# Kernel tuning notes

Hardware: AMD Instinct MI355X
Metric: run time of the kernel (lower is better)

Reference implementation:

```python
import jax, jax.numpy as jnp
import numpy as np

N_NODES = 50000
N_EDGES = 800000
D = 128


def _dense_params(key, d_in, d_out):
    kw, kb = jax.random.split(key)
    W = jax.random.normal(kw, (d_in, d_out), dtype=jnp.float32) / np.sqrt(d_in)
    b = jnp.zeros((d_out,), dtype=jnp.float32)
    return W, b


def setup_inputs() -> dict:
    key = jax.random.key(0)
    ks = jax.random.split(key, 9)
    nodes = jax.random.normal(ks[0], (N_NODES, D), dtype=jnp.float32)
    edges = jax.random.normal(ks[1], (N_EDGES, D), dtype=jnp.float32)
    senders = jax.random.randint(ks[2], (N_EDGES,), 0, N_NODES, dtype=jnp.int32)
    receivers = jax.random.randint(ks[3], (N_EDGES,), 0, N_NODES, dtype=jnp.int32)
    W_s1, b_s1 = _dense_params(ks[4], D, D)   # Dense on nodes -> sent_attributes_1
    W_r, b_r = _dense_params(ks[5], D, D)     # Dense on nodes -> received_attributes
    W_e, b_e = _dense_params(ks[6], D, D)     # Dense on edges
    W_att, b_att = _dense_params(ks[7], D, 1) # attention Dense -> scalar per edge
    W_m, b_m = _dense_params(ks[8], D, D)     # Dense on message (simple_update)
    return {
        "nodes": nodes, "edges": edges, "senders": senders, "receivers": receivers,
        "W_s1": W_s1, "b_s1": b_s1, "W_r": W_r, "b_r": b_r,
        "W_e": W_e, "b_e": b_e, "W_att": W_att, "b_att": b_att,
        "W_m": W_m, "b_m": b_m,
    }


def reference(nodes, edges, senders, receivers,
              W_s1, b_s1, W_r, b_r, W_e, b_e, W_att, b_att, W_m, b_m):
    n = nodes.shape[0]
    # dense projections on nodes, then gather along edges
    sent_1 = (nodes @ W_s1 + b_s1)[senders]          # [E, D]
    received = (nodes @ W_r + b_r)[receivers]        # [E, D]
    sent_2 = nodes[senders]                          # [E, D] (simple_update: raw gather)
    e_proj = edges @ W_e + b_e                       # [E, D]
    edges_new = sent_1 + e_proj + received           # add_features=True
    # attention: Dense(1) + leaky_relu, segment softmax over receivers
    att = jax.nn.leaky_relu(edges_new @ W_att + b_att)          # [E, 1]
    seg_max = jax.ops.segment_max(att, receivers, num_segments=n)
    expv = jnp.exp(att - seg_max[receivers])
    denom = jax.ops.segment_sum(expv, receivers, num_segments=n)
    weights = expv / denom[receivers]                            # [E, 1]
    # message: Dense on gathered sender features, weighted scatter-sum
    message = weights * (sent_2 @ W_m + b_m)                     # [E, D]
    nodes_new = jax.ops.segment_sum(message, receivers, num_segments=n)  # [N, D]
    return nodes_new, edges_new
```

## Files before the change

### kernel.cpp

```cpp
#include <hip/hip_runtime.h>
#include <hip/hip_bf16.h>
#include <cstdint>
#include <cstddef>

#define NN 50000
#define NE 800000
#define DD 128

typedef __attribute__((ext_vector_type(8))) short short8;
typedef __attribute__((ext_vector_type(4))) float f32x4;

__device__ __forceinline__ unsigned short f2bf(float f) {
  unsigned u = __float_as_uint(f);
  u = (u + 0x7FFFu + ((u >> 16) & 1u)) >> 16;
  return (unsigned short)u;
}

__global__ void k_prep(const float* __restrict__ Ws1, const float* __restrict__ Wr,
                       const float* __restrict__ Wm, const float* __restrict__ We,
                       unsigned short* __restrict__ Wt) {
  int i = blockIdx.x * blockDim.x + threadIdx.x;
  for (int idx = i; idx < 4 * DD * DD; idx += gridDim.x * blockDim.x) {
    int m = idx >> 14, r = idx & 16383, col = r >> 7, k = r & 127;
    const float* src = (m == 0) ? Ws1 : (m == 1) ? Wr : (m == 2) ? Wm : We;
    Wt[idx] = f2bf(src[k * DD + col]);
  }
}

__device__ __forceinline__ unsigned cvtpk(float lo, float hi) {
  unsigned r;
  asm("v_cvt_pk_bf16_f32 %0, %1, %2" : "=v"(r) : "v"(lo), "v"(hi));
  return r;
}

__device__ __forceinline__ short8 cvt8(f32x4 f0, f32x4 f1) {
  union { short8 s; unsigned u[4]; } t;
  t.u[0] = cvtpk(f0[0], f0[1]);
  t.u[1] = cvtpk(f0[2], f0[3]);
  t.u[2] = cvtpk(f1[0], f1[1]);
  t.u[3] = cvtpk(f1[2], f1[3]);
  return t.s;
}

__device__ __forceinline__ void stage_w(const unsigned short* __restrict__ Wt,
                                        char* __restrict__ lds, int tid) {
#pragma unroll
  for (int c = 0; c < 8; ++c) {
    int ci = tid * 8 + c;
    int col = ci >> 4, slot = ci & 15;
    uint4 v = *(const uint4*)(Wt + ci * 8);
    *(uint4*)(lds + col * 256 + ((slot ^ col) & 15) * 16) = v;
  }
}

__device__ __forceinline__ short8 read_w(const char* __restrict__ lds, int col, int slot) {
  return *(const short8*)(lds + col * 256 + ((slot ^ col) & 15) * 16);
}

__global__ __launch_bounds__(256, 4) void k_nodeproj(
    const float* __restrict__ nodes, const unsigned short* __restrict__ Wt,
    const float* __restrict__ b_s1, const float* __restrict__ b_r, const float* __restrict__ b_m,
    float* __restrict__ P1, float* __restrict__ Pr, float* __restrict__ Pm) {
  __shared__ char ldsW[32768];
  int m = blockIdx.y;
  int tid = threadIdx.x;
  stage_w(Wt + m * 16384, ldsW, tid);
  __syncthreads();
  const float* bias = (m == 0) ? b_s1 : (m == 1) ? b_r : b_m;
  float* P = (m == 0) ? P1 : (m == 1) ? Pr : Pm;
  int wid = tid >> 6, l = tid & 63;
  int lmod = l & 15, ldiv = l >> 4;
  int wave = blockIdx.x * 4 + wid, nw = gridDim.x * 4;
  for (int b = wave; b < NN / 16; b += nw) {
    int row = b * 16 + lmod;
    const float* nrow = nodes + (size_t)row * DD;
    short8 bb[4];
#pragma unroll
    for (int kk = 0; kk < 4; ++kk) {
      const f32x4* p = (const f32x4*)(nrow + kk * 32 + ldiv * 8);
      bb[kk] = cvt8(p[0], p[1]);
    }
    f32x4 acc[8] = {};
#pragma unroll
    for (int kk = 0; kk < 4; ++kk) {
#pragma unroll
      for (int rb = 0; rb < 8; ++rb) {
        short8 a = read_w(ldsW, rb * 16 + lmod, kk * 4 + ldiv);
        acc[rb] = __builtin_amdgcn_mfma_f32_16x16x32_bf16(a, bb[kk], acc[rb], 0, 0, 0);
      }
    }
    float* Prow = P + (size_t)row * DD;
#pragma unroll
    for (int rb = 0; rb < 8; ++rb) {
      int d0 = rb * 16 + ldiv * 4;
      f32x4 bv = *(const f32x4*)(bias + d0);
      f32x4 v = acc[rb];
#pragma unroll
      for (int j = 0; j < 4; ++j) v[j] += bv[j];
      *(f32x4*)(Prow + d0) = v;
    }
  }
}

__global__ __launch_bounds__(256, 4) void k_edge(
    const float* __restrict__ edges, const int* __restrict__ senders,
    const int* __restrict__ receivers, const unsigned short* __restrict__ WtE,
    const float* __restrict__ b_e, const float* __restrict__ P1, const float* __restrict__ Pr,
    const float* __restrict__ W_att, const float* __restrict__ b_att,
    float* __restrict__ out_edges, float* __restrict__ attb, int* __restrict__ cnt) {
  __shared__ char ldsW[32768];
  int tid = threadIdx.x;
  stage_w(WtE, ldsW, tid);
  __syncthreads();
  int wid = tid >> 6, l = tid & 63;
  int lmod = l & 15, ldiv = l >> 4;
  int wave = blockIdx.x * 4 + wid, nw = gridDim.x * 4;
  float batt = b_att[0];
  for (int b = wave; b < NE / 16; b += nw) {
    int e = b * 16 + lmod;
    const float* erow = edges + (size_t)e * DD;
    short8 bb[4];
#pragma unroll
    for (int kk = 0; kk < 4; ++kk) {
      const f32x4* p = (const f32x4*)(erow + kk * 32 + ldiv * 8);
      f32x4 f0 = __builtin_nontemporal_load(p);
      f32x4 f1 = __builtin_nontemporal_load(p + 1);
      bb[kk] = cvt8(f0, f1);
    }
    f32x4 acc[8] = {};
#pragma unroll
    for (int kk = 0; kk < 4; ++kk) {
#pragma unroll
      for (int rb = 0; rb < 8; ++rb) {
        short8 a = read_w(ldsW, rb * 16 + lmod, kk * 4 + ldiv);
        acc[rb] = __builtin_amdgcn_mfma_f32_16x16x32_bf16(a, bb[kk], acc[rb], 0, 0, 0);
      }
    }
    int s = senders[e], rc = receivers[e];
    const float* p1 = P1 + (size_t)s * DD;
    const float* pr = Pr + (size_t)rc * DD;
    float* oe = out_edges + (size_t)e * DD;
    float att = 0.f;
#pragma unroll
    for (int rb = 0; rb < 8; ++rb) {
      int d0 = rb * 16 + ldiv * 4;
      f32x4 g1 = *(const f32x4*)(p1 + d0);
      f32x4 gr = *(const f32x4*)(pr + d0);
      f32x4 be = *(const f32x4*)(b_e + d0);
      f32x4 wa = *(const f32x4*)(W_att + d0);
      f32x4 v = acc[rb];
#pragma unroll
      for (int j = 0; j < 4; ++j) {
        float x = v[j] + be[j] + g1[j] + gr[j];
        v[j] = x;
        att += x * wa[j];
      }
      __builtin_nontemporal_store(v, (f32x4*)(oe + d0));
    }
    att += __shfl_xor(att, 16);
    att += __shfl_xor(att, 32);
    if (ldiv == 0) {
      float av = att + batt;
      av = (av >= 0.f) ? av : 0.01f * av;
      attb[e] = av;
      atomicAdd(&cnt[rc], 1);
    }
  }
}

__global__ __launch_bounds__(1024) void k_scan(const int* __restrict__ cnt,
                                               int* __restrict__ offs) {
  __shared__ int wsum[16];
  __shared__ int sbase;
  int t = threadIdx.x;
  int lane = t & 63, wid = t >> 6;
  if (t == 0) { sbase = 0; offs[0] = 0; }
  __syncthreads();
  for (int c = 0; c < 13; ++c) {
    int i0 = c * 4096 + t * 4;
    int v0 = 0, v1 = 0, v2 = 0, v3 = 0;
    if (i0 + 3 < NN) {
      int4 v = *(const int4*)(cnt + i0);
      v0 = v.x; v1 = v.y; v2 = v.z; v3 = v.w;
    } else {
      if (i0 + 0 < NN) v0 = cnt[i0 + 0];
      if (i0 + 1 < NN) v1 = cnt[i0 + 1];
      if (i0 + 2 < NN) v2 = cnt[i0 + 2];
      if (i0 + 3 < NN) v3 = cnt[i0 + 3];
    }
    int p1 = v0, p2 = p1 + v1, p3 = p2 + v2, p4 = p3 + v3;
    int x = p4;
#pragma unroll
    for (int d = 1; d < 64; d <<= 1) {
      int o = __shfl_up(x, d, 64);
      if (lane >= d) x += o;
    }
    if (lane == 63) wsum[wid] = x;
    int excl_lane = x - p4;
    __syncthreads();
    int wbase = 0, tot = 0;
#pragma unroll
    for (int w2 = 0; w2 < 16; ++w2) {
      int sv = wsum[w2];
      if (w2 < wid) wbase += sv;
      tot += sv;
    }
    int base = sbase + wbase + excl_lane;
    if (i0 + 0 < NN) offs[i0 + 1] = base + p1;
    if (i0 + 1 < NN) offs[i0 + 2] = base + p2;
    if (i0 + 2 < NN) offs[i0 + 3] = base + p3;
    if (i0 + 3 < NN) offs[i0 + 4] = base + p4;
    __syncthreads();
    if (t == 0) sbase += tot;
    __syncthreads();
  }
}

__global__ void k_fill(const int* __restrict__ receivers, const int* __restrict__ offs,
                       int* __restrict__ cursor, int* __restrict__ eidx) {
  int e = blockIdx.x * 256 + threadIdx.x;
  if (e < NE) {
    int rc = receivers[e];
    int pos = offs[rc] + atomicAdd(&cursor[rc], 1);
    eidx[pos] = e;
  }
}

__global__ __launch_bounds__(256) void k_node(
    const int* __restrict__ offs, const int* __restrict__ eidx,
    const int* __restrict__ senders, const float* __restrict__ attb,
    const float* __restrict__ Pm, float* __restrict__ out_nodes) {
  int wid = threadIdx.x >> 6, l = threadIdx.x & 63;
  int n = blockIdx.x * 4 + wid;
  if (n >= NN) return;
  int start = offs[n], end = offs[n + 1];
  float m = -3.4e38f, denom = 0.f, ax = 0.f, ay = 0.f;
  for (int c = start; c < end; c += 64) {
    int rem = end - c;
    if (rem > 64) rem = 64;
    float a_l = -3.4e38f;
    int s_l = 0;
    if (l < rem) {
      int e = eidx[c + l];
      a_l = attb[e];
      s_l = senders[e];
    }
    float cm = a_l;
#pragma unroll
    for (int d = 1; d < 64; d <<= 1) cm = fmaxf(cm, __shfl_xor(cm, d));
    if (cm > m) {
      float sc = __expf(m - cm);
      denom *= sc; ax *= sc; ay *= sc;
      m = cm;
    }
#pragma unroll 4
    for (int i = 0; i < rem; ++i) {
      float a = __shfl(a_l, i);
      int s = __shfl(s_l, i);
      float w = __expf(a - m);
      denom += w;
      float2 v = *(const float2*)(Pm + (size_t)s * DD + l * 2);
      ax += w * v.x;
      ay += w * v.y;
    }
  }
  float2 o = {0.f, 0.f};
  if (end > start) {
    float inv = 1.f / denom;
    o.x = ax * inv;
    o.y = ay * inv;
  }
  *(float2*)(out_nodes + (size_t)n * DD + l * 2) = o;
}

extern "C" void kernel_launch(void* const* d_in, const int* in_sizes, int n_in,
                              void* d_out, int out_size, void* d_ws, size_t ws_size,
                              hipStream_t stream) {
  (void)in_sizes; (void)n_in; (void)out_size; (void)ws_size;
  const float* nodes = (const float*)d_in[0];
  const float* edges = (const float*)d_in[1];
  const int* senders = (const int*)d_in[2];
  const int* receivers = (const int*)d_in[3];
  const float* W_s1 = (const float*)d_in[4];
  const float* b_s1 = (const float*)d_in[5];
  const float* W_r = (const float*)d_in[6];
  const float* b_r = (const float*)d_in[7];
  const float* W_e = (const float*)d_in[8];
  const float* b_e = (const float*)d_in[9];
  const float* W_att = (const float*)d_in[10];
  const float* b_att = (const float*)d_in[11];
  const float* W_m = (const float*)d_in[12];
  const float* b_m = (const float*)d_in[13];

  float* out_nodes = (float*)d_out;
  float* out_edges = out_nodes + (size_t)NN * DD;

  char* w = (char*)d_ws;
  unsigned short* Wt = (unsigned short*)w; w += (size_t)4 * DD * DD * 2;
  float* P1 = (float*)w; w += (size_t)NN * DD * 4;
  float* Pr = (float*)w; w += (size_t)NN * DD * 4;
  float* Pm = (float*)w; w += (size_t)NN * DD * 4;
  float* attb = (float*)w; w += (size_t)NE * 4;
  int* eidx = (int*)w; w += (size_t)NE * 4;
  int* cnt = (int*)w; w += (size_t)NN * 4;
  int* cursor = (int*)w; w += (size_t)NN * 4;
  int* offs = (int*)w; w += (size_t)(NN + 1) * 4;

  hipMemsetAsync(cnt, 0, (size_t)NN * 8, stream);

  k_prep<<<64, 256, 0, stream>>>(W_s1, W_r, W_m, W_e, Wt);
  k_nodeproj<<<dim3(256, 3), 256, 0, stream>>>(nodes, Wt, b_s1, b_r, b_m, P1, Pr, Pm);
  k_edge<<<1024, 256, 0, stream>>>(edges, senders, receivers, Wt + 3 * 16384, b_e,
                                   P1, Pr, W_att, b_att, out_edges, attb, cnt);
  k_scan<<<1, 1024, 0, stream>>>(cnt, offs);
  k_fill<<<(NE + 255) / 256, 256, 0, stream>>>(receivers, offs, cursor, eidx);
  k_node<<<NN / 4, 256, 0, stream>>>(offs, eidx, senders, attb, Pm, out_nodes);
}
```

Before: 456.3 us.

## Prefetch next edge tile in k_edge and fold edge bias into P1

The edge kernel now software-pipelines its loop: while the MFMA work runs on the current 16-edge tile, the raw edge rows and sender/receiver indices for the next tile are loaded into registers. The edge bias b_e is added into the P1 node projection, which removes one per-edge vector load. Launch bounds and grid size for k_edge go from 4 to 5 blocks per CU and from 1024 to 1280 blocks, and the inner aggregation loop in k_node is unrolled 8 instead of 4. The extra prefetch registers compete with the higher occupancy target and could cause spills.

```diff
diff --git a/kernel.cpp b/kernel.cpp
--- a/kernel.cpp
+++ b/kernel.cpp
@@ -60,6 +60,7 @@
 __global__ __launch_bounds__(256, 4) void k_nodeproj(
     const float* __restrict__ nodes, const unsigned short* __restrict__ Wt,
     const float* __restrict__ b_s1, const float* __restrict__ b_r, const float* __restrict__ b_m,
+    const float* __restrict__ b_e,
     float* __restrict__ P1, float* __restrict__ Pr, float* __restrict__ Pm) {
   __shared__ char ldsW[32768];
   int m = blockIdx.y;
@@ -94,6 +95,11 @@
     for (int rb = 0; rb < 8; ++rb) {
       int d0 = rb * 16 + ldiv * 4;
       f32x4 bv = *(const f32x4*)(bias + d0);
+      if (m == 0) {
+        f32x4 be = *(const f32x4*)(b_e + d0);
+#pragma unroll
+        for (int j = 0; j < 4; ++j) bv[j] += be[j];
+      }
       f32x4 v = acc[rb];
 #pragma unroll
       for (int j = 0; j < 4; ++j) v[j] += bv[j];
@@ -102,10 +108,10 @@
   }
 }
 
-__global__ __launch_bounds__(256, 4) void k_edge(
+__global__ __launch_bounds__(256, 5) void k_edge(
     const float* __restrict__ edges, const int* __restrict__ senders,
     const int* __restrict__ receivers, const unsigned short* __restrict__ WtE,
-    const float* __restrict__ b_e, const float* __restrict__ P1, const float* __restrict__ Pr,
+    const float* __restrict__ P1, const float* __restrict__ Pr,
     const float* __restrict__ W_att, const float* __restrict__ b_att,
     float* __restrict__ out_edges, float* __restrict__ attb, int* __restrict__ cnt) {
   __shared__ char ldsW[32768];
@@ -115,17 +121,35 @@
   int wid = tid >> 6, l = tid & 63;
   int lmod = l & 15, ldiv = l >> 4;
   int wave = blockIdx.x * 4 + wid, nw = gridDim.x * 4;
+  const int NB = NE / 16;
   float batt = b_att[0];
-  for (int b = wave; b < NE / 16; b += nw) {
+
+  int b = wave;
+  if (b >= NB) return;
+  f32x4 cur[8];
+  int s, rc;
+  {
     int e = b * 16 + lmod;
-    const float* erow = edges + (size_t)e * DD;
+    const f32x4* erow = (const f32x4*)(edges + (size_t)e * DD);
+#pragma unroll
+    for (int q = 0; q < 8; ++q) cur[q] = __builtin_nontemporal_load(erow + ((q >> 1) * 8 + ldiv * 2 + (q & 1)));
+    s = senders[e];
+    rc = receivers[e];
+  }
+
+  while (b < NB) {
+    int bn = b + nw;
     short8 bb[4];
 #pragma unroll
-    for (int kk = 0; kk < 4; ++kk) {
-      const f32x4* p = (const f32x4*)(erow + kk * 32 + ldiv * 8);
-      f32x4 f0 = __builtin_nontemporal_load(p);
-      f32x4 f1 = __builtin_nontemporal_load(p + 1);
-      bb[kk] = cvt8(f0, f1);
+    for (int kk = 0; kk < 4; ++kk) bb[kk] = cvt8(cur[2 * kk], cur[2 * kk + 1]);
+    int s0 = s, rc0 = rc;
+    if (bn < NB) {
+      int en = bn * 16 + lmod;
+      const f32x4* erow = (const f32x4*)(edges + (size_t)en * DD);
+#pragma unroll
+      for (int q = 0; q < 8; ++q) cur[q] = __builtin_nontemporal_load(erow + ((q >> 1) * 8 + ldiv * 2 + (q & 1)));
+      s = senders[en];
+      rc = receivers[en];
     }
     f32x4 acc[8] = {};
 #pragma unroll
@@ -136,9 +160,9 @@
         acc[rb] = __builtin_amdgcn_mfma_f32_16x16x32_bf16(a, bb[kk], acc[rb], 0, 0, 0);
       }
     }
-    int s = senders[e], rc = receivers[e];
-    const float* p1 = P1 + (size_t)s * DD;
-    const float* pr = Pr + (size_t)rc * DD;
+    int e = b * 16 + lmod;
+    const float* p1 = P1 + (size_t)s0 * DD;
+    const float* pr = Pr + (size_t)rc0 * DD;
     float* oe = out_edges + (size_t)e * DD;
     float att = 0.f;
 #pragma unroll
@@ -146,12 +170,11 @@
       int d0 = rb * 16 + ldiv * 4;
       f32x4 g1 = *(const f32x4*)(p1 + d0);
       f32x4 gr = *(const f32x4*)(pr + d0);
-      f32x4 be = *(const f32x4*)(b_e + d0);
       f32x4 wa = *(const f32x4*)(W_att + d0);
       f32x4 v = acc[rb];
 #pragma unroll
       for (int j = 0; j < 4; ++j) {
-        float x = v[j] + be[j] + g1[j] + gr[j];
+        float x = v[j] + g1[j] + gr[j];
         v[j] = x;
         att += x * wa[j];
       }
@@ -163,8 +186,9 @@
       float av = att + batt;
       av = (av >= 0.f) ? av : 0.01f * av;
       attb[e] = av;
-      atomicAdd(&cnt[rc], 1);
-    }
+      atomicAdd(&cnt[rc0], 1);
+    }
+    b = bn;
   }
 }
 
@@ -253,7 +277,7 @@
       denom *= sc; ax *= sc; ay *= sc;
       m = cm;
     }
-#pragma unroll 4
+#pragma unroll 8
     for (int i = 0; i < rem; ++i) {
       float a = __shfl(a_l, i);
       int s = __shfl(s_l, i);
@@ -309,8 +333,8 @@
   hipMemsetAsync(cnt, 0, (size_t)NN * 8, stream);
 
   k_prep<<<64, 256, 0, stream>>>(W_s1, W_r, W_m, W_e, Wt);
-  k_nodeproj<<<dim3(256, 3), 256, 0, stream>>>(nodes, Wt, b_s1, b_r, b_m, P1, Pr, Pm);
-  k_edge<<<1024, 256, 0, stream>>>(edges, senders, receivers, Wt + 3 * 16384, b_e,
+  k_nodeproj<<<dim3(256, 3), 256, 0, stream>>>(nodes, Wt, b_s1, b_r, b_m, b_e, P1, Pr, Pm);
+  k_edge<<<1280, 256, 0, stream>>>(edges, senders, receivers, Wt + 3 * 16384,
                                    P1, Pr, W_att, b_att, out_edges, attb, cnt);
   k_scan<<<1, 1024, 0, stream>>>(cnt, offs);
   k_fill<<<(NE + 255) / 256, 256, 0, stream>>>(receivers, offs, cursor, eidx);
```

Measured after the change: 576.2 us. +26.3%, slower.
